# Kernel optimization log

Measured on AMD Instinct MI355X. Metric: run time of the kernel, lower is better.

Reference implementation:

```python
import jax, jax.numpy as jnp
import numpy as np

DT = 0.01
REG = 0.01

def setup_inputs() -> dict:
    key = jax.random.key(0)
    k1, k2, k3, k4 = jax.random.split(key, 4)
    B, C_in, L = 16, 128, 4096
    C_out, KS = 256, 9
    return {
        "x": jax.random.normal(k1, (B, C_in, L), dtype=jnp.float32),
        "weight": jax.random.normal(k2, (C_out, C_in, KS), dtype=jnp.float32) * np.sqrt(2.0 / (C_out * KS)),
        "bias": jnp.zeros((C_out,), dtype=jnp.float32),
        "vel": jax.random.normal(k3, (C_in, KS), dtype=jnp.float32) * 0.1,
        "acc": jax.random.normal(k4, (C_in, KS), dtype=jnp.float32) * 0.01,
        "ks": 9,
        "stride": 1,
        "pad": 4,
    }

def reference(x, weight, bias, vel, acc, ks, stride, pad):
    # x: [B, C_in, L]
    if pad > 0:
        x = jnp.pad(x, ((0, 0), (0, 0), (pad, pad)), mode="edge")  # replicate pad
    L_pad = x.shape[2]
    L_out = (L_pad - ks) // stride + 1
    t_off = jnp.arange(ks, dtype=jnp.float32) * DT  # [ks]
    # unfold: gather sliding windows -> [B, C_in, L_out, ks]
    idx = jnp.arange(L_out)[:, None] * stride + jnp.arange(ks)[None, :]
    xu = x[:, :, idx]
    # per-tap physics offset: vel*t + 0.5*acc*t^2, shape [C_in, ks] broadcast
    offset = vel * t_off + 0.5 * acc * (t_off ** 2)  # [C_in, ks]
    xt = xu + offset[None, :, None, :]  # [B, C_in, L_out, ks]
    # GEMM: [B, L_out, C_in*ks] x [C_in*ks, C_out]
    out = jnp.einsum("bclk,ock->bol", xt, weight) + bias[None, :, None]
    phys = REG * (jnp.mean(vel ** 2) + jnp.mean(acc ** 2))
    return (out, phys)
```

## Files before the change

kernel.cpp:

```cpp
#include <hip/hip_runtime.h>
#include <hip/hip_bf16.h>

typedef unsigned short u16;
typedef __bf16 bf16x8 __attribute__((ext_vector_type(8)));
typedef float f32x4 __attribute__((ext_vector_type(4)));
typedef unsigned short ushort8 __attribute__((ext_vector_type(8)));

#define C_IN   128
#define C_OUT  256
#define BATCH  16
#define LEN    4096
#define KS     9
#define PAD    4
#define LPAD   (LEN + 2*PAD)
#define KTOT   (C_IN * KS)
#define NSTEP  36

__device__ inline u16 f2bf(float f) {
    __hip_bfloat16 h = __float2bfloat16(f);
    return __builtin_bit_cast(u16, h);
}

__device__ __forceinline__ void g2l16(const void* g, void* l) {
    __builtin_amdgcn_global_load_lds(
        (const __attribute__((address_space(1))) void*)g,
        (__attribute__((address_space(3))) void*)l, 16, 0, 0);
}

__global__ void prep_xt(const float* __restrict__ x, u16* __restrict__ xt) {
    int b    = blockIdx.y;
    int lane = threadIdx.x & 63;
    int jb   = threadIdx.x >> 6;
    int lp   = blockIdx.x * 64 + lane;
    if (lp >= LPAD) return;
    int l = lp - PAD;
    l = l < 0 ? 0 : (l > LEN - 1 ? LEN - 1 : l);
    const float* xb = x + (size_t)b * C_IN * LEN + l;
    u16* row = xt + ((size_t)b * LPAD + lp) * C_IN;
    int key = lp & 15;
    #pragma unroll
    for (int jj = 0; jj < 4; ++jj) {
        int cblk = jb * 4 + jj;
        ushort8 v;
        #pragma unroll
        for (int e = 0; e < 8; ++e)
            v[e] = f2bf(xb[(size_t)(cblk * 8 + e) * LEN]);
        int jstore = cblk ^ key;
        *reinterpret_cast<ushort8*>(row + jstore * 8) = v;
    }
}

__global__ void prep_wb(const float* __restrict__ w, const float* __restrict__ bias,
                        const float* __restrict__ vel, const float* __restrict__ acc,
                        u16* __restrict__ w4, float* __restrict__ ebias,
                        float* __restrict__ phys_out) {
    int t = threadIdx.x;
    if (blockIdx.x < 1152) {
        int i = blockIdx.x * 256 + t;
        int e  = i & 7;
        int r  = i >> 3;
        int mr = r & 15;
        int kg = (r >> 4) & 3;
        int ob = (r >> 6) & 15;
        int s  = r >> 10;
        int o  = ob * 16 + mr;
        int k  = s >> 2;
        int c  = (s & 3) * 32 + kg * 8 + e;
        w4[i] = f2bf(w[((size_t)o * C_IN + c) * KS + k]);
        return;
    }
    __shared__ float red[256];
    int o = blockIdx.x - 1152;
    float sum = 0.f;
    for (int i = t; i < KTOT; i += 256) {
        int k = i % KS;
        float tk = k * 0.01f;
        float off = vel[i] * tk + 0.5f * acc[i] * tk * tk;
        sum += off * w[(size_t)o * KTOT + i];
    }
    red[t] = sum;
    __syncthreads();
    for (int h = 128; h > 0; h >>= 1) {
        if (t < h) red[t] += red[t + h];
        __syncthreads();
    }
    if (t == 0) ebias[o] = bias[o] + red[0];

    if (o == 0) {
        __syncthreads();
        float pv = 0.f;
        for (int i = t; i < KTOT; i += 256) {
            float v = vel[i], a = acc[i];
            pv += v * v + a * a;
        }
        red[t] = pv;
        __syncthreads();
        for (int h = 128; h > 0; h >>= 1) {
            if (t < h) red[t] += red[t + h];
            __syncthreads();
        }
        if (t == 0) *phys_out = 0.01f * (red[0] / (float)KTOT);
    }
}

__global__ __launch_bounds__(256, 2) void conv_main(const u16* __restrict__ xt,
                                                    const u16* __restrict__ w4,
                                                    const float* __restrict__ ebias,
                                                    float* __restrict__ out) {
    __shared__ u16 ldsx[17408];
    __shared__ u16 ldsa[4][4096];

    int b     = blockIdx.z;
    int obase = blockIdx.y * 128;
    int lbase = blockIdx.x * 128;
    int t     = threadIdx.x;
    int lane  = t & 63;
    int w     = t >> 6;
    int wm    = w >> 1;
    int wn    = w & 1;
    int mrow  = lane & 15;
    int kgrp  = lane >> 4;

    const u16* asrc = w4 + (size_t)(obase >> 4) * 512;

    {
        const u16* bsrc = xt + ((size_t)b * LPAD + lbase) * C_IN;
        #pragma unroll
        for (int j = 0; j < 8; ++j)
            g2l16(bsrc + (j * 256 + t) * 8, ldsx + (j * 256 + w * 64) * 8);
        if (t < 128)
            g2l16(bsrc + (2048 + t) * 8, ldsx + (2048 + w * 64) * 8);
        #pragma unroll
        for (int p = 0; p < 3; ++p)
            #pragma unroll
            for (int j = 0; j < 2; ++j)
                g2l16(asrc + (size_t)p * 8192 + (j * 256 + t) * 8,
                      ldsa[p] + (j * 256 + w * 64) * 8);
    }
    __syncthreads();

    f32x4 acc[4][4] = {};
    const char* ldsbase = reinterpret_cast<const char*>(ldsx);
    int afoff = (wm << 12) + lane * 16;

    #define LOAD_A_BUF(BUF, AF)                                                  \
        {                                                                        \
            const char* ab_ = reinterpret_cast<const char*>(ldsa[BUF]) + afoff;  \
            _Pragma("unroll")                                                    \
            for (int mi = 0; mi < 4; ++mi)                                       \
                AF[mi] = *reinterpret_cast<const bf16x8*>(ab_ + (mi << 10));     \
        }
    #define LOAD_B(S, BF)                                                        \
        {                                                                        \
            int k_ = (S) >> 2;                                                   \
            int coff_ = ((S) & 3) * 64 + kgrp * 16;                              \
            _Pragma("unroll")                                                    \
            for (int ni = 0; ni < 4; ++ni) {                                     \
                int row_  = wn * 64 + ni * 16 + mrow + k_;                       \
                int addr_ = row_ * 256 + coff_;                                  \
                addr_ ^= (row_ & 15) << 4;                                       \
                BF[ni] = *reinterpret_cast<const bf16x8*>(ldsbase + addr_);      \
            }                                                                    \
        }
    #define STAGE_A(S, BUF)                                                      \
        {                                                                        \
            const u16* as_ = asrc + (size_t)(S) * 8192;                          \
            _Pragma("unroll")                                                    \
            for (int j = 0; j < 2; ++j)                                          \
                g2l16(as_ + (j * 256 + t) * 8, ldsa[BUF] + (j * 256 + w * 64) * 8); \
        }
    #define MFMA16(AF, BF)                                                       \
        {                                                                        \
            _Pragma("unroll")                                                    \
            for (int ni = 0; ni < 4; ++ni)                                       \
                _Pragma("unroll")                                                \
                for (int mi = 0; mi < 4; ++mi)                                   \
                    acc[mi][ni] = __builtin_amdgcn_mfma_f32_16x16x32_bf16(       \
                        AF[mi], BF[ni], acc[mi][ni], 0, 0, 0);                   \
        }

    bf16x8 ar[2][4], br[2][4];
    LOAD_A_BUF(0, ar[0]);
    LOAD_B(0, br[0]);

    #pragma unroll
    for (int s = 0; s < NSTEP; ++s) {
        const int cur = s & 1, nx = cur ^ 1;
        if (s + 3 < NSTEP) STAGE_A(s + 3, (s + 3) & 3);
        if (s + 1 < NSTEP) { LOAD_A_BUF((s + 1) & 3, ar[nx]); LOAD_B(s + 1, br[nx]); }
        MFMA16(ar[cur], br[cur]);
        if (s + 1 < NSTEP) {
            if (s + 3 < NSTEP) asm volatile("s_waitcnt vmcnt(2)" ::: "memory");
            else               asm volatile("s_waitcnt vmcnt(0)" ::: "memory");
            asm volatile("s_waitcnt lgkmcnt(0)" ::: "memory");
            __builtin_amdgcn_s_barrier();
        }
    }

    #pragma unroll
    for (int mi = 0; mi < 4; ++mi) {
        int o0 = obase + wm * 64 + mi * 16 + kgrp * 4;
        f32x4 eb = *reinterpret_cast<const f32x4*>(ebias + o0);
        #pragma unroll
        for (int ni = 0; ni < 4; ++ni) {
            int l = lbase + wn * 64 + ni * 16 + mrow;
            float* op = out + (size_t)(b * C_OUT + o0) * LEN + l;
            #pragma unroll
            for (int r = 0; r < 4; ++r)
                op[(size_t)r * LEN] = acc[mi][ni][r] + eb[r];
        }
    }
    #undef LOAD_A_BUF
    #undef LOAD_B
    #undef STAGE_A
    #undef MFMA16
}

extern "C" void kernel_launch(void* const* d_in, const int* in_sizes, int n_in,
                              void* d_out, int out_size, void* d_ws, size_t ws_size,
                              hipStream_t stream) {
    const float* x      = (const float*)d_in[0];
    const float* weight = (const float*)d_in[1];
    const float* bias   = (const float*)d_in[2];
    const float* vel    = (const float*)d_in[3];
    const float* acc    = (const float*)d_in[4];
    float* out = (float*)d_out;

    char* ws = (char*)d_ws;
    u16*  xt    = (u16*)ws;
    u16*  w4    = (u16*)(ws + (size_t)BATCH * LPAD * C_IN * 2);
    float* ebias = (float*)(ws + (size_t)BATCH * LPAD * C_IN * 2 + (size_t)C_OUT * KTOT * 2);

    hipLaunchKernelGGL(prep_xt, dim3((LPAD + 63) / 64, BATCH), dim3(256), 0, stream, x, xt);
    hipLaunchKernelGGL(prep_wb, dim3(1152 + 256), dim3(256), 0, stream,
                       weight, bias, vel, acc, w4, ebias, out + (size_t)BATCH * C_OUT * LEN);
    hipLaunchKernelGGL(conv_main, dim3(LEN / 128, C_OUT / 128, BATCH), dim3(256), 0, stream,
                       xt, w4, ebias, out);
}
```

Baseline: 61.30 us.

## Cover all output channels per block and merge prep kernels into one launch

The conv kernel now computes all 256 output channels per block (8x4 MFMA tiles per wave) instead of splitting channels across two blocks. This halves the grid and reuses each staged input tile across twice as many weights, so the input tile is loaded into LDS half as often. The weight pipeline drops from a 4-deep, 3-ahead prefetch with register double-buffering to 2 LDS buffers with a full wait each step. The two preprocessing kernels are merged into one launch. The costs are higher register pressure from 128 accumulators, less latency hiding, and fewer blocks (512) to fill the GPU.

```diff
diff --git a/kernel.cpp b/kernel.cpp
--- a/kernel.cpp
+++ b/kernel.cpp
@@ -16,6 +16,10 @@
 #define KTOT   (C_IN * KS)
 #define NSTEP  36
 
+#define XT_BLKS    1040
+#define W4_BLKS    1152
+#define EB_BLKS    256
+
 __device__ inline u16 f2bf(float f) {
     __hip_bfloat16 h = __float2bfloat16(f);
     return __builtin_bit_cast(u16, h);
@@ -27,36 +31,39 @@
         (__attribute__((address_space(3))) void*)l, 16, 0, 0);
 }
 
-__global__ void prep_xt(const float* __restrict__ x, u16* __restrict__ xt) {
-    int b    = blockIdx.y;
-    int lane = threadIdx.x & 63;
-    int jb   = threadIdx.x >> 6;
-    int lp   = blockIdx.x * 64 + lane;
-    if (lp >= LPAD) return;
-    int l = lp - PAD;
-    l = l < 0 ? 0 : (l > LEN - 1 ? LEN - 1 : l);
-    const float* xb = x + (size_t)b * C_IN * LEN + l;
-    u16* row = xt + ((size_t)b * LPAD + lp) * C_IN;
-    int key = lp & 15;
-    #pragma unroll
-    for (int jj = 0; jj < 4; ++jj) {
-        int cblk = jb * 4 + jj;
-        ushort8 v;
-        #pragma unroll
-        for (int e = 0; e < 8; ++e)
-            v[e] = f2bf(xb[(size_t)(cblk * 8 + e) * LEN]);
-        int jstore = cblk ^ key;
-        *reinterpret_cast<ushort8*>(row + jstore * 8) = v;
-    }
-}
-
-__global__ void prep_wb(const float* __restrict__ w, const float* __restrict__ bias,
-                        const float* __restrict__ vel, const float* __restrict__ acc,
-                        u16* __restrict__ w4, float* __restrict__ ebias,
-                        float* __restrict__ phys_out) {
+__global__ void prep_all(const float* __restrict__ x, const float* __restrict__ w,
+                         const float* __restrict__ bias, const float* __restrict__ vel,
+                         const float* __restrict__ acc_in,
+                         u16* __restrict__ xt, u16* __restrict__ w4,
+                         float* __restrict__ ebias, float* __restrict__ phys_out) {
+    int bid = blockIdx.x;
     int t = threadIdx.x;
-    if (blockIdx.x < 1152) {
-        int i = blockIdx.x * 256 + t;
+    if (bid < XT_BLKS) {
+        int b    = bid / 65;
+        int lblk = bid % 65;
+        int lane = t & 63;
+        int jb   = t >> 6;
+        int lp   = lblk * 64 + lane;
+        if (lp >= LPAD) return;
+        int l = lp - PAD;
+        l = l < 0 ? 0 : (l > LEN - 1 ? LEN - 1 : l);
+        const float* xb = x + (size_t)b * C_IN * LEN + l;
+        u16* row = xt + ((size_t)b * LPAD + lp) * C_IN;
+        int key = lp & 15;
+        #pragma unroll
+        for (int jj = 0; jj < 4; ++jj) {
+            int cblk = jb * 4 + jj;
+            ushort8 v;
+            #pragma unroll
+            for (int e = 0; e < 8; ++e)
+                v[e] = f2bf(xb[(size_t)(cblk * 8 + e) * LEN]);
+            int jstore = cblk ^ key;
+            *reinterpret_cast<ushort8*>(row + jstore * 8) = v;
+        }
+        return;
+    }
+    if (bid < XT_BLKS + W4_BLKS) {
+        int i = (bid - XT_BLKS) * 256 + t;
         int e  = i & 7;
         int r  = i >> 3;
         int mr = r & 15;
@@ -70,12 +77,12 @@
         return;
     }
     __shared__ float red[256];
-    int o = blockIdx.x - 1152;
+    int o = bid - (XT_BLKS + W4_BLKS);
     float sum = 0.f;
     for (int i = t; i < KTOT; i += 256) {
         int k = i % KS;
         float tk = k * 0.01f;
-        float off = vel[i] * tk + 0.5f * acc[i] * tk * tk;
+        float off = vel[i] * tk + 0.5f * acc_in[i] * tk * tk;
         sum += off * w[(size_t)o * KTOT + i];
     }
     red[t] = sum;
@@ -90,7 +97,7 @@
         __syncthreads();
         float pv = 0.f;
         for (int i = t; i < KTOT; i += 256) {
-            float v = vel[i], a = acc[i];
+            float v = vel[i], a = acc_in[i];
             pv += v * v + a * a;
         }
         red[t] = pv;
@@ -108,10 +115,9 @@
                                                     const float* __restrict__ ebias,
                                                     float* __restrict__ out) {
     __shared__ u16 ldsx[17408];
-    __shared__ u16 ldsa[4][4096];
-
-    int b     = blockIdx.z;
-    int obase = blockIdx.y * 128;
+    __shared__ u16 ldsa[2][8192];
+
+    int b     = blockIdx.y;
     int lbase = blockIdx.x * 128;
     int t     = threadIdx.x;
     int lane  = t & 63;
@@ -121,8 +127,6 @@
     int mrow  = lane & 15;
     int kgrp  = lane >> 4;
 
-    const u16* asrc = w4 + (size_t)(obase >> 4) * 512;
-
     {
         const u16* bsrc = xt + ((size_t)b * LPAD + lbase) * C_IN;
         #pragma unroll
@@ -131,23 +135,20 @@
         if (t < 128)
             g2l16(bsrc + (2048 + t) * 8, ldsx + (2048 + w * 64) * 8);
         #pragma unroll
-        for (int p = 0; p < 3; ++p)
-            #pragma unroll
-            for (int j = 0; j < 2; ++j)
-                g2l16(asrc + (size_t)p * 8192 + (j * 256 + t) * 8,
-                      ldsa[p] + (j * 256 + w * 64) * 8);
+        for (int j = 0; j < 4; ++j)
+            g2l16(w4 + (j * 256 + t) * 8, ldsa[0] + (j * 256 + w * 64) * 8);
     }
     __syncthreads();
 
-    f32x4 acc[4][4] = {};
+    f32x4 acc[8][4] = {};
     const char* ldsbase = reinterpret_cast<const char*>(ldsx);
-    int afoff = (wm << 12) + lane * 16;
+    int afoff = (wm << 13) + lane * 16;
 
     #define LOAD_A_BUF(BUF, AF)                                                  \
         {                                                                        \
             const char* ab_ = reinterpret_cast<const char*>(ldsa[BUF]) + afoff;  \
             _Pragma("unroll")                                                    \
-            for (int mi = 0; mi < 4; ++mi)                                       \
+            for (int mi = 0; mi < 8; ++mi)                                       \
                 AF[mi] = *reinterpret_cast<const bf16x8*>(ab_ + (mi << 10));     \
         }
     #define LOAD_B(S, BF)                                                        \
@@ -164,42 +165,33 @@
         }
     #define STAGE_A(S, BUF)                                                      \
         {                                                                        \
-            const u16* as_ = asrc + (size_t)(S) * 8192;                          \
+            const u16* as_ = w4 + (size_t)(S) * 8192;                            \
             _Pragma("unroll")                                                    \
-            for (int j = 0; j < 2; ++j)                                          \
+            for (int j = 0; j < 4; ++j)                                          \
                 g2l16(as_ + (j * 256 + t) * 8, ldsa[BUF] + (j * 256 + w * 64) * 8); \
         }
-    #define MFMA16(AF, BF)                                                       \
-        {                                                                        \
-            _Pragma("unroll")                                                    \
-            for (int ni = 0; ni < 4; ++ni)                                       \
-                _Pragma("unroll")                                                \
-                for (int mi = 0; mi < 4; ++mi)                                   \
-                    acc[mi][ni] = __builtin_amdgcn_mfma_f32_16x16x32_bf16(       \
-                        AF[mi], BF[ni], acc[mi][ni], 0, 0, 0);                   \
-        }
-
-    bf16x8 ar[2][4], br[2][4];
-    LOAD_A_BUF(0, ar[0]);
-    LOAD_B(0, br[0]);
 
     #pragma unroll
     for (int s = 0; s < NSTEP; ++s) {
-        const int cur = s & 1, nx = cur ^ 1;
-        if (s + 3 < NSTEP) STAGE_A(s + 3, (s + 3) & 3);
-        if (s + 1 < NSTEP) { LOAD_A_BUF((s + 1) & 3, ar[nx]); LOAD_B(s + 1, br[nx]); }
-        MFMA16(ar[cur], br[cur]);
+        if (s + 1 < NSTEP) STAGE_A(s + 1, (s + 1) & 1);
+        bf16x8 af[8], bf[4];
+        LOAD_A_BUF(s & 1, af);
+        LOAD_B(s, bf);
+        #pragma unroll
+        for (int mi = 0; mi < 8; ++mi)
+            #pragma unroll
+            for (int ni = 0; ni < 4; ++ni)
+                acc[mi][ni] = __builtin_amdgcn_mfma_f32_16x16x32_bf16(
+                    af[mi], bf[ni], acc[mi][ni], 0, 0, 0);
         if (s + 1 < NSTEP) {
-            if (s + 3 < NSTEP) asm volatile("s_waitcnt vmcnt(2)" ::: "memory");
-            else               asm volatile("s_waitcnt vmcnt(0)" ::: "memory");
-            asm volatile("s_waitcnt lgkmcnt(0)" ::: "memory");
+            asm volatile("s_waitcnt vmcnt(0) lgkmcnt(0)" ::: "memory");
             __builtin_amdgcn_s_barrier();
         }
     }
 
     #pragma unroll
-    for (int mi = 0; mi < 4; ++mi) {
-        int o0 = obase + wm * 64 + mi * 16 + kgrp * 4;
+    for (int mi = 0; mi < 8; ++mi) {
+        int o0 = wm * 128 + mi * 16 + kgrp * 4;
         f32x4 eb = *reinterpret_cast<const f32x4*>(ebias + o0);
         #pragma unroll
         for (int ni = 0; ni < 4; ++ni) {
@@ -213,7 +205,6 @@
     #undef LOAD_A_BUF
     #undef LOAD_B
     #undef STAGE_A
-    #undef MFMA16
 }
 
 extern "C" void kernel_launch(void* const* d_in, const int* in_sizes, int n_in,
@@ -231,9 +222,9 @@
     u16*  w4    = (u16*)(ws + (size_t)BATCH * LPAD * C_IN * 2);
     float* ebias = (float*)(ws + (size_t)BATCH * LPAD * C_IN * 2 + (size_t)C_OUT * KTOT * 2);
 
-    hipLaunchKernelGGL(prep_xt, dim3((LPAD + 63) / 64, BATCH), dim3(256), 0, stream, x, xt);
-    hipLaunchKernelGGL(prep_wb, dim3(1152 + 256), dim3(256), 0, stream,
-                       weight, bias, vel, acc, w4, ebias, out + (size_t)BATCH * C_OUT * LEN);
-    hipLaunchKernelGGL(conv_main, dim3(LEN / 128, C_OUT / 128, BATCH), dim3(256), 0, stream,
+    hipLaunchKernelGGL(prep_all, dim3(XT_BLKS + W4_BLKS + EB_BLKS), dim3(256), 0, stream,
+                       x, weight, bias, vel, acc, xt, w4, ebias,
+                       out + (size_t)BATCH * C_OUT * LEN);
+    hipLaunchKernelGGL(conv_main, dim3(LEN / 128, BATCH), dim3(256), 0, stream,
                        xt, w4, ebias, out);
 }
```

After: 58.57 us. -4.4%, faster.
